# Kernel tuning notes

Hardware: AMD Instinct MI355X
Metric: run time of the kernel (lower is better)

Reference implementation:

```python
import jax, jax.numpy as jnp
import numpy as np

E = 8        # num_experts
K = 2        # top_k routing
D = 1024     # d_model
F = 4096     # expert hidden (ffn) dim
EPS = 1e-5


def _layernorm(h, g, b):
    # h: [E, T, C]; g, b: [E, C]
    mu = h.mean(axis=-1, keepdims=True)
    var = ((h - mu) ** 2).mean(axis=-1, keepdims=True)
    return (h - mu) * jax.lax.rsqrt(var + EPS) * g[:, None, :] + b[:, None, :]


def setup_inputs() -> dict:
    key = jax.random.key(0)
    ks = jax.random.split(key, 8)
    B, S = 2, 2048
    x = jax.random.normal(ks[0], (B, S, D), dtype=jnp.float32)
    Wr = jax.random.normal(ks[1], (D, E), dtype=jnp.float32) / np.sqrt(D)
    br = jnp.zeros((E,), dtype=jnp.float32)
    W1 = jax.random.normal(ks[2], (E, D, F), dtype=jnp.float32) / np.sqrt(D)
    b1 = jnp.zeros((E, F), dtype=jnp.float32)
    g1 = jnp.ones((E, F), dtype=jnp.float32)
    be1 = jnp.zeros((E, F), dtype=jnp.float32)
    W2 = jax.random.normal(ks[3], (E, F, D), dtype=jnp.float32) / np.sqrt(F)
    b2 = jnp.zeros((E, D), dtype=jnp.float32)
    g2 = jnp.ones((E, D), dtype=jnp.float32)
    be2 = jnp.zeros((E, D), dtype=jnp.float32)
    return {"x": x, "Wr": Wr, "br": br, "W1": W1, "b1": b1, "g1": g1,
            "be1": be1, "W2": W2, "b2": b2, "g2": g2, "be2": be2}


def reference(x, Wr, br, W1, b1, g1, be1, W2, b2, g2, be2):
    B, S, _ = x.shape
    xt = x.reshape(-1, D)                       # [T, D] token matrix
    # --- router + sampler: top-k softmax probs, renormalized over the k slots
    logits = xt @ Wr + br                       # [T, E]
    p = jax.nn.softmax(logits, axis=-1)
    probs, idx = jax.lax.top_k(p, K)            # [T, K]
    probs = probs / probs.sum(axis=-1, keepdims=True)
    # --- experts layer 1: Linear -> relu -> LayerNorm, per expert
    h = jnp.einsum('td,edf->etf', xt, W1) + b1[:, None, :]   # [E, T, F]
    h = _layernorm(jax.nn.relu(h), g1, be1)
    # --- experts layer 2: Linear -> relu -> LayerNorm
    y = jnp.einsum('etf,efd->etd', h, W2) + b2[:, None, :]   # [E, T, D]
    y = _layernorm(jax.nn.relu(y), g2, be2)
    # --- weighted scatter-combine: gate[t,e] = sum_k 1[idx[t,k]==e] * probs[t,k]
    gate = (jax.nn.one_hot(idx, E, dtype=x.dtype) * probs[..., None]).sum(axis=1)  # [T, E]
    out = jnp.einsum('te,etd->td', gate, y)     # index_add combine, dense form
    return out.reshape(B, S, D)
```

## Files before the change

### kernel.cpp

```cpp
#include <hip/hip_runtime.h>


#define E_N 8
#define TOPK 2
#define DM 1024
#define FF 4096
#define NTOK 4096
#define NA 8192
#define LN_EPS 1e-5f
#define NBX 128

typedef __attribute__((ext_vector_type(4))) float f32x4;
typedef __attribute__((ext_vector_type(8))) short short8;

__device__ __forceinline__ unsigned short f2bf(float f) {
    unsigned int u = __builtin_bit_cast(unsigned int, f);
    u = (u + 0x7FFFu + ((u >> 16) & 1u)) >> 16;
    return (unsigned short)u;
}
__device__ __forceinline__ float bf2f(unsigned short h) {
    unsigned int u = ((unsigned int)h) << 16;
    return __builtin_bit_cast(float, u);
}
__device__ __forceinline__ void unp(unsigned int u, float& lo, float& hi) {
    lo = bf2f((unsigned short)(u & 0xffffu));
    hi = bf2f((unsigned short)(u >> 16));
}
__device__ __forceinline__ unsigned int pk(float lo, float hi) {
    return (unsigned int)f2bf(lo) | ((unsigned int)f2bf(hi) << 16);
}

__device__ __forceinline__ void gload16(const unsigned short* g, unsigned short* lds) {
    __builtin_amdgcn_global_load_lds(
        (const __attribute__((address_space(1))) unsigned int*)g,
        (__attribute__((address_space(3))) unsigned int*)lds, 16, 0, 0);
}

__device__ __forceinline__ void stage_tile(const float* __restrict__ s, int sld,
                                           float* buf) {
    int tid = threadIdx.x;
    int wv = tid >> 6, lane = tid & 63;
    int kl = lane >> 5;
    int n = (lane & 31) * 4;
#pragma unroll
    for (int i = 0; i < 8; i++) {
        int j = wv * 8 + i;
        int k = j * 2 + kl;
        gload16((const unsigned short*)(s + (size_t)k * sld + n),
                (unsigned short*)(buf + j * 256));
    }
}

__device__ __forceinline__ void emit_tile(const float* __restrict__ tile,
                                          unsigned short* __restrict__ out) {
    int tid = threadIdx.x;
    int r = tid >> 1, gh = (tid & 1) * 4;
    const float* col = tile + r;
    unsigned int ov[16];
#pragma unroll
    for (int i = 0; i < 4; i++) {
        int kb = ((gh + i) ^ (r & 7)) << 3;
#pragma unroll
        for (int ee = 0; ee < 8; ee += 2)
            ov[i * 4 + (ee >> 1)] = pk(col[(kb + ee) * 128], col[(kb + ee + 1) * 128]);
    }
    unsigned short* dp = out + (size_t)r * 64 + gh * 8;
#pragma unroll
    for (int i = 0; i < 4; i++)
        *(uint4*)(dp + i * 8) = *(uint4*)&ov[i * 4];
}


__global__ __launch_bounds__(256) void k_prep(
        const float* __restrict__ W1, const float* __restrict__ W2,
        unsigned short* __restrict__ W1T, unsigned short* __restrict__ W2T,
        const float* __restrict__ x, const float* __restrict__ Wr,
        const float* __restrict__ br, unsigned short* __restrict__ xb,
        int* __restrict__ topk_idx, float* __restrict__ topk_p)
{
    __shared__ float tile[2][64 * 128];
    int bid = blockIdx.x;
    int tid = threadIdx.x;

    if (bid >= 2048) {
        int blk = bid - 2048;
        int wv = tid >> 6, lane = tid & 63;
        int t = blk * 4 + wv;
        const float* xr = x + (size_t)t * DM;
        unsigned short* xbr = xb + (size_t)t * DM;
        float4 xv[4];
#pragma unroll
        for (int p = 0; p < 4; p++)
            xv[p] = *(const float4*)(xr + p * 256 + lane * 4);
#pragma unroll
        for (int p = 0; p < 4; p++) {
            uint2 pkd; pkd.x = pk(xv[p].x, xv[p].y); pkd.y = pk(xv[p].z, xv[p].w);
            *(uint2*)(xbr + p * 256 + lane * 4) = pkd;
        }
        float a0=0,a1=0,a2=0,a3=0,a4=0,a5=0,a6=0,a7=0;
#pragma unroll
        for (int p = 0; p < 4; p++) {
            int d0 = p * 256 + lane * 4;
            float xs[4] = {xv[p].x, xv[p].y, xv[p].z, xv[p].w};
#pragma unroll
            for (int j = 0; j < 4; j++) {
                const float4* wp = (const float4*)(Wr + (d0 + j) * 8);
                float4 w0 = wp[0], w1 = wp[1];
                a0 += xs[j] * w0.x; a1 += xs[j] * w0.y; a2 += xs[j] * w0.z; a3 += xs[j] * w0.w;
                a4 += xs[j] * w1.x; a5 += xs[j] * w1.y; a6 += xs[j] * w1.z; a7 += xs[j] * w1.w;
            }
        }
#pragma unroll
        for (int off = 32; off; off >>= 1) {
            a0 += __shfl_xor(a0, off); a1 += __shfl_xor(a1, off);
            a2 += __shfl_xor(a2, off); a3 += __shfl_xor(a3, off);
            a4 += __shfl_xor(a4, off); a5 += __shfl_xor(a5, off);
            a6 += __shfl_xor(a6, off); a7 += __shfl_xor(a7, off);
        }
        if (lane == 0) {
            float l[8] = {a0 + br[0], a1 + br[1], a2 + br[2], a3 + br[3],
                          a4 + br[4], a5 + br[5], a6 + br[6], a7 + br[7]};
            int i0 = 0;
#pragma unroll
            for (int e = 1; e < 8; e++) if (l[e] > l[i0]) i0 = e;
            int i1 = (i0 == 0) ? 1 : 0;
#pragma unroll
            for (int e = 0; e < 8; e++) if (e != i0 && l[e] > l[i1]) i1 = e;
            float p1 = expf(l[i1] - l[i0]);
            float s = 1.0f + p1;
            topk_idx[2 * t]     = i0;
            topk_idx[2 * t + 1] = i1;
            topk_p[2 * t]       = 1.0f / s;
            topk_p[2 * t + 1]   = p1 / s;
        }
        return;
    }

    const float* s; unsigned short* o; int sld;
    if (bid < 1024) {
        int z = bid >> 7, nt = (bid >> 2) & 31, kt0 = (bid & 3) * 4;
        s = W1 + (size_t)z * DM * FF + (size_t)(kt0 * 64) * FF + nt * 128;
        sld = FF;
        o = W1T + (((size_t)z * 32 + nt) * 16 + kt0) * 8192;
    } else {
        int b = bid - 1024;
        int e = b >> 7, nt = (b >> 4) & 7, kt0 = (b & 15) * 4;
        s = W2 + (size_t)e * FF * DM + (size_t)(kt0 * 64) * DM + nt * 128;
        sld = DM;
        o = W2T + (((size_t)e * 8 + nt) * 64 + kt0) * 8192;
    }

    stage_tile(s, sld, tile[0]);
    __syncthreads();
#pragma unroll
    for (int q = 0; q < 4; q++) {
        if (q < 3)
            stage_tile(s + (size_t)(q + 1) * 64 * sld, sld, tile[(q + 1) & 1]);
        emit_tile(tile[q & 1], o + (size_t)q * 8192);
        if (q < 3) __syncthreads();
    }
}


__global__ __launch_bounds__(256) void k_route2(const int* __restrict__ topk_idx,
        int* __restrict__ cnt, int* __restrict__ offs,
        int* __restrict__ assign_tok, int* __restrict__ assign_e,
        int* __restrict__ slot)
{
    __shared__ int h[8], base[8];
    int tid = threadIdx.x;
    if (tid < 8) h[tid] = 0;
    __syncthreads();
    int el[32];
#pragma unroll
    for (int i = 0; i < 32; i++) {
        int idx = tid * 32 + i;
        el[i] = topk_idx[idx];
        atomicAdd(&h[el[i]], 1);
    }
    __syncthreads();
    if (tid == 0) {
        int s = 0;
        for (int e = 0; e < E_N; e++) { offs[e] = s; cnt[e] = h[e]; base[e] = s; s += h[e]; }
        offs[E_N] = s;
    }
    __syncthreads();
    if (tid < 8) h[tid] = base[tid];
    __syncthreads();
#pragma unroll
    for (int i = 0; i < 32; i++) {
        int idx = tid * 32 + i;
        int e = el[i];
        int pos = atomicAdd(&h[e], 1);
        assign_tok[pos] = idx >> 1;
        assign_e[pos] = e;
        slot[idx] = pos;
    }
}


template<bool GATHER, bool EPI>
__global__ __launch_bounds__(256, 4) void k_gemm(
    const unsigned short* __restrict__ A,
    const unsigned short* __restrict__ BT,
    const float* __restrict__ bias,
    unsigned short* __restrict__ C,
    const int* __restrict__ cnt, const int* __restrict__ offs,
    const int* __restrict__ gather_tok,
    int Kslice, int N, int ldA, int NT, int KT, int GX, int KS, size_t slicePitch)
{
    __shared__ __align__(1024) char lds[32768];

    int bid = blockIdx.x;
    int e = bid & 7;
    int lb = bid >> 3;
    int M = cnt[e];
    if (M <= 0) return;
    int off_e = offs[e];
    int nrows = (M + 127) >> 7;
    int ntiles = nrows * GX * KS;

    int tid = threadIdx.x;
    int wv = tid >> 6, lane = tid & 63;
    int lr = lane & 15, hi = lane >> 4;
    int mW = (wv >> 1) * 64, nW = (wv & 1) * 64;
    int colsw = ((lane & 7) ^ (lane >> 3)) * 8;
    int l3 = lane >> 3;
    int nt = Kslice >> 6;

    for (int t = lb; t < ntiles; t += NBX) {
        int r = t % nrows;
        int q = t / nrows;
        int xn = q % GX;
        int ks = q / GX;
        int m0 = r * 128;
        int n0 = xn * 128;
        int kbase = ks * Kslice;

        const unsigned short* aptr[4];
        const unsigned short* bptr[4];
        size_t btile = ((size_t)(e * NT + xn) * KT + (size_t)ks * nt) * 8192;
#pragma unroll
        for (int i = 0; i < 4; i++) {
            int j = wv * 4 + i;
            int rr = m0 + j * 8 + l3; rr = (rr < M) ? rr : (M - 1);
            size_t arow = GATHER ? (size_t)gather_tok[off_e + rr] : (size_t)(off_e + rr);
            aptr[i] = A + arow * (size_t)ldA + kbase + colsw;
            bptr[i] = BT + btile + j * 512 + lane * 8;
        }

        f32x4 acc[4][4];
        f32x4 zz = {0.f, 0.f, 0.f, 0.f};
#pragma unroll
        for (int mi = 0; mi < 4; mi++)
#pragma unroll
            for (int ni = 0; ni < 4; ni++) acc[mi][ni] = zz;

        for (int kt = 0; kt < nt; ++kt) {
            __syncthreads();
#pragma unroll
            for (int i = 0; i < 4; i++) {
                gload16(aptr[i] + kt * 64, (unsigned short*)(lds + (wv * 4 + i) * 1024));
                gload16(bptr[i] + (size_t)kt * 8192,
                        (unsigned short*)(lds + 16384 + (wv * 4 + i) * 1024));
            }
            __syncthreads();
#pragma unroll
            for (int kss = 0; kss < 2; kss++) {
                int cb = (kss * 64 + hi * 16) ^ ((lr & 7) << 4);
                short8 afr[4], bfr[4];
#pragma unroll
                for (int ni = 0; ni < 4; ni++)
                    bfr[ni] = *(const short8*)(lds + 16384 + (nW + ni * 16 + lr) * 128 + cb);
#pragma unroll
                for (int mi = 0; mi < 4; mi++)
                    afr[mi] = *(const short8*)(lds + (mW + mi * 16 + lr) * 128 + cb);
                __builtin_amdgcn_s_setprio(1);
#pragma unroll
                for (int mi = 0; mi < 4; mi++)
#pragma unroll
                    for (int ni = 0; ni < 4; ni++)
                        acc[mi][ni] = __builtin_amdgcn_mfma_f32_16x16x32_bf16(
                            afr[mi], bfr[ni], acc[mi][ni], 0, 0, 0);
                __builtin_amdgcn_s_setprio(0);
            }
        }

        unsigned short* Cs = C + ks * slicePitch;
        float bv[4] = {0.f, 0.f, 0.f, 0.f};
        if (EPI) {
#pragma unroll
            for (int ni = 0; ni < 4; ni++)
                bv[ni] = bias[(size_t)e * N + (n0 + nW + ni * 16 + lr)];
        }
#pragma unroll
        for (int mi = 0; mi < 4; mi++) {
            int mb = m0 + mW + mi * 16 + hi * 4;
#pragma unroll
            for (int rr = 0; rr < 4; rr++) {
                int m = mb + rr;
                if (m < M) {
                    unsigned short* crow = Cs + (size_t)(off_e + m) * N;
#pragma unroll
                    for (int ni = 0; ni < 4; ni++) {
                        float v = acc[mi][ni][rr];
                        if (EPI) v = fmaxf(v + bv[ni], 0.0f);
                        crow[n0 + nW + ni * 16 + lr] = f2bf(v);
                    }
                }
            }
        }
    }
}


__global__ __launch_bounds__(256) void k_ln1(unsigned short* __restrict__ H,
        const float* __restrict__ g, const float* __restrict__ b,
        const int* __restrict__ assign_e)
{
    size_t a = blockIdx.x;
    int e = assign_e[a];
    unsigned short* row = H + a * FF;
    int tid = threadIdx.x;
    uint4 u0 = *(const uint4*)(row + tid * 16);
    uint4 u1 = *(const uint4*)(row + tid * 16 + 8);
    float v[16];
    unp(u0.x, v[0], v[1]);  unp(u0.y, v[2], v[3]);
    unp(u0.z, v[4], v[5]);  unp(u0.w, v[6], v[7]);
    unp(u1.x, v[8], v[9]);  unp(u1.y, v[10], v[11]);
    unp(u1.z, v[12], v[13]); unp(u1.w, v[14], v[15]);
    float s = 0.f, q = 0.f;
#pragma unroll
    for (int i = 0; i < 16; i++) { s += v[i]; q += v[i] * v[i]; }
#pragma unroll
    for (int off = 32; off; off >>= 1) { s += __shfl_xor(s, off); q += __shfl_xor(q, off); }
    __shared__ float red[8];
    int wv = tid >> 6, lane = tid & 63;
    if (lane == 0) { red[wv * 2] = s; red[wv * 2 + 1] = q; }
    __syncthreads();
    s = red[0] + red[2] + red[4] + red[6];
    q = red[1] + red[3] + red[5] + red[7];
    float mu = s * (1.0f / FF);
    float var = q * (1.0f / FF) - mu * mu;
    float rstd = rsqrtf(var + LN_EPS);
    const float* gg = g + (size_t)e * FF + tid * 16;
    const float* bb = b + (size_t)e * FF + tid * 16;
    float4 G0 = *(const float4*)(gg);      float4 G1 = *(const float4*)(gg + 4);
    float4 G2 = *(const float4*)(gg + 8);  float4 G3 = *(const float4*)(gg + 12);
    float4 B0 = *(const float4*)(bb);      float4 B1 = *(const float4*)(bb + 4);
    float4 B2 = *(const float4*)(bb + 8);  float4 B3 = *(const float4*)(bb + 12);
    float gvv[16] = {G0.x,G0.y,G0.z,G0.w,G1.x,G1.y,G1.z,G1.w,G2.x,G2.y,G2.z,G2.w,G3.x,G3.y,G3.z,G3.w};
    float bvv[16] = {B0.x,B0.y,B0.z,B0.w,B1.x,B1.y,B1.z,B1.w,B2.x,B2.y,B2.z,B2.w,B3.x,B3.y,B3.z,B3.w};
#pragma unroll
    for (int i = 0; i < 16; i++) v[i] = (v[i] - mu) * rstd * gvv[i] + bvv[i];
    u0.x = pk(v[0], v[1]);  u0.y = pk(v[2], v[3]);
    u0.z = pk(v[4], v[5]);  u0.w = pk(v[6], v[7]);
    u1.x = pk(v[8], v[9]);  u1.y = pk(v[10], v[11]);
    u1.z = pk(v[12], v[13]); u1.w = pk(v[14], v[15]);
    *(uint4*)(row + tid * 16) = u0;
    *(uint4*)(row + tid * 16 + 8) = u1;
}


__global__ __launch_bounds__(256) void k_comb(const unsigned short* __restrict__ Yp,
        const float* __restrict__ g, const float* __restrict__ b2,
        const float* __restrict__ be,
        const int* __restrict__ slot, const float* __restrict__ topk_p,
        const int* __restrict__ assign_e, float* __restrict__ out)
{
    int t = blockIdx.x;
    int s0 = slot[2 * t], s1 = slot[2 * t + 1];
    float p0 = topk_p[2 * t], p1 = topk_p[2 * t + 1];
    int e0 = assign_e[s0], e1 = assign_e[s1];
    int tid = threadIdx.x;
    int d = tid * 4;
    const unsigned short* Y1 = Yp + (size_t)NA * DM;
    uint2 ua0 = *(const uint2*)(Yp + (size_t)s0 * DM + d);
    uint2 ua1 = *(const uint2*)(Y1 + (size_t)s0 * DM + d);
    uint2 ub0 = *(const uint2*)(Yp + (size_t)s1 * DM + d);
    uint2 ub1 = *(const uint2*)(Y1 + (size_t)s1 * DM + d);
    float4 bza = *(const float4*)(b2 + (size_t)e0 * DM + d);
    float4 bzb = *(const float4*)(b2 + (size_t)e1 * DM + d);
    float x0, x1, y0, y1;
    float va[4], vb[4];
    unp(ua0.x, x0, x1); unp(ua1.x, y0, y1);
    va[0] = fmaxf(x0 + y0 + bza.x, 0.f); va[1] = fmaxf(x1 + y1 + bza.y, 0.f);
    unp(ua0.y, x0, x1); unp(ua1.y, y0, y1);
    va[2] = fmaxf(x0 + y0 + bza.z, 0.f); va[3] = fmaxf(x1 + y1 + bza.w, 0.f);
    unp(ub0.x, x0, x1); unp(ub1.x, y0, y1);
    vb[0] = fmaxf(x0 + y0 + bzb.x, 0.f); vb[1] = fmaxf(x1 + y1 + bzb.y, 0.f);
    unp(ub0.y, x0, x1); unp(ub1.y, y0, y1);
    vb[2] = fmaxf(x0 + y0 + bzb.z, 0.f); vb[3] = fmaxf(x1 + y1 + bzb.w, 0.f);

    float sa = 0.f, qa = 0.f, sb = 0.f, qb = 0.f;
#pragma unroll
    for (int i = 0; i < 4; i++) {
        sa += va[i]; qa += va[i] * va[i];
        sb += vb[i]; qb += vb[i] * vb[i];
    }
#pragma unroll
    for (int off = 32; off; off >>= 1) {
        sa += __shfl_xor(sa, off); qa += __shfl_xor(qa, off);
        sb += __shfl_xor(sb, off); qb += __shfl_xor(qb, off);
    }
    __shared__ float red[16];
    int wv = tid >> 6, lane = tid & 63;
    if (lane == 0) { red[wv*4+0]=sa; red[wv*4+1]=qa; red[wv*4+2]=sb; red[wv*4+3]=qb; }
    __syncthreads();
    sa = red[0] + red[4] + red[8]  + red[12];
    qa = red[1] + red[5] + red[9]  + red[13];
    sb = red[2] + red[6] + red[10] + red[14];
    qb = red[3] + red[7] + red[11] + red[15];
    float mua = sa * (1.0f / DM), vara = qa * (1.0f / DM) - mua * mua;
    float ra = rsqrtf(vara + LN_EPS);
    float mub = sb * (1.0f / DM), varb = qb * (1.0f / DM) - mub * mub;
    float rb = rsqrtf(varb + LN_EPS);
    float4 ga  = *(const float4*)(g + (size_t)e0 * DM + d);
    float4 ba  = *(const float4*)(be + (size_t)e0 * DM + d);
    float4 gb4 = *(const float4*)(g + (size_t)e1 * DM + d);
    float4 bb4 = *(const float4*)(be + (size_t)e1 * DM + d);
    float4 o;
    o.x = p0 * ((va[0] - mua) * ra * ga.x + ba.x) + p1 * ((vb[0] - mub) * rb * gb4.x + bb4.x);
    o.y = p0 * ((va[1] - mua) * ra * ga.y + ba.y) + p1 * ((vb[1] - mub) * rb * gb4.y + bb4.y);
    o.z = p0 * ((va[2] - mua) * ra * ga.z + ba.z) + p1 * ((vb[2] - mub) * rb * gb4.z + bb4.z);
    o.w = p0 * ((va[3] - mua) * ra * ga.w + ba.w) + p1 * ((vb[3] - mub) * rb * gb4.w + bb4.w);
    *(float4*)(out + (size_t)t * DM + d) = o;
}


extern "C" void kernel_launch(void* const* d_in, const int* in_sizes, int n_in,
                              void* d_out, int out_size, void* d_ws, size_t ws_size,
                              hipStream_t stream) {
    const float* x   = (const float*)d_in[0];
    const float* Wr  = (const float*)d_in[1];
    const float* br  = (const float*)d_in[2];
    const float* W1  = (const float*)d_in[3];
    const float* b1  = (const float*)d_in[4];
    const float* g1  = (const float*)d_in[5];
    const float* be1 = (const float*)d_in[6];
    const float* W2  = (const float*)d_in[7];
    const float* b2  = (const float*)d_in[8];
    const float* g2  = (const float*)d_in[9];
    const float* be2 = (const float*)d_in[10];
    float* out = (float*)d_out;

    char* w = (char*)d_ws;
    int*   cnt        = (int*)(w);
    int*   offs       = (int*)(w + 128);
    int*   topk_idx   = (int*)(w + 512);
    float* topk_p     = (float*)(w + 512 + (32 << 10));
    int*   assign_tok = (int*)(w + 512 + (64 << 10));
    int*   assign_e   = (int*)(w + 512 + (96 << 10));
    int*   slot       = (int*)(w + 512 + (128 << 10));
    unsigned short* xb  = (unsigned short*)(w + ((size_t)1 << 20));
    unsigned short* W1T = (unsigned short*)(w + ((size_t)9 << 20));
    unsigned short* W2T = (unsigned short*)(w + ((size_t)73 << 20));
    unsigned short* Hb  = (unsigned short*)(w + ((size_t)137 << 20));
    unsigned short* Yp  = (unsigned short*)(w + ((size_t)201 << 20));

    k_prep<<<3072, 256, 0, stream>>>(
        W1, W2, W1T, W2T, x, Wr, br, xb, topk_idx, topk_p);
    k_route2<<<1, 256, 0, stream>>>(topk_idx, cnt, offs, assign_tok, assign_e, slot);
    k_gemm<true, true><<<8 * NBX, 256, 0, stream>>>(
        xb, W1T, b1, Hb, cnt, offs, assign_tok, DM, FF, DM, 32, 16, 32, 1, 0);
    k_ln1<<<NA, 256, 0, stream>>>(Hb, g1, be1, assign_e);
    k_gemm<false, false><<<8 * NBX, 256, 0, stream>>>(
        Hb, W2T, nullptr, Yp, cnt, offs, nullptr, FF / 2, DM, FF, 8, 64, 8, 2,
        (size_t)NA * DM);
    k_comb<<<NTOK, 256, 0, stream>>>(Yp, g2, b2, be2, slot, topk_p, assign_e, out);
}
```

Baseline: 333.4 us.

## Fuse W2 transpose/convert into first expert GEMM to overlap with compute

Moves the fp32-to-bf16 transposed packing of W2 out of the prep kernel and into the first grouped GEMM. Its 512 tiles per expert are interleaved evenly among that expert's GEMM tiles, so the memory-bound weight conversion can overlap with MFMA work. This shrinks the prep kernel but adds extra syncthreads, LDS reuse and divergent work inside the GEMM's persistent loop. If an expert has zero tokens, that expert's W2T is never written.

After: 346.9 us. 1.04x slower.

```diff
diff --git a/kernel.cpp b/kernel.cpp
--- a/kernel.cpp
+++ b/kernel.cpp
@@ -72,8 +72,7 @@
 
 
 __global__ __launch_bounds__(256) void k_prep(
-        const float* __restrict__ W1, const float* __restrict__ W2,
-        unsigned short* __restrict__ W1T, unsigned short* __restrict__ W2T,
+        const float* __restrict__ W1, unsigned short* __restrict__ W1T,
         const float* __restrict__ x, const float* __restrict__ Wr,
         const float* __restrict__ br, unsigned short* __restrict__ xb,
         int* __restrict__ topk_idx, float* __restrict__ topk_p)
@@ -82,8 +81,8 @@
     int bid = blockIdx.x;
     int tid = threadIdx.x;
 
-    if (bid >= 2048) {
-        int blk = bid - 2048;
+    if (bid >= 1024) {
+        int blk = bid - 1024;
         int wv = tid >> 6, lane = tid & 63;
         int t = blk * 4 + wv;
         const float* xr = x + (size_t)t * DM;
@@ -136,26 +135,16 @@
         return;
     }
 
-    const float* s; unsigned short* o; int sld;
-    if (bid < 1024) {
-        int z = bid >> 7, nt = (bid >> 2) & 31, kt0 = (bid & 3) * 4;
-        s = W1 + (size_t)z * DM * FF + (size_t)(kt0 * 64) * FF + nt * 128;
-        sld = FF;
-        o = W1T + (((size_t)z * 32 + nt) * 16 + kt0) * 8192;
-    } else {
-        int b = bid - 1024;
-        int e = b >> 7, nt = (b >> 4) & 7, kt0 = (b & 15) * 4;
-        s = W2 + (size_t)e * FF * DM + (size_t)(kt0 * 64) * DM + nt * 128;
-        sld = DM;
-        o = W2T + (((size_t)e * 8 + nt) * 64 + kt0) * 8192;
-    }
-
-    stage_tile(s, sld, tile[0]);
+    int z = bid >> 7, nt = (bid >> 2) & 31, kt0 = (bid & 3) * 4;
+    const float* s = W1 + (size_t)z * DM * FF + (size_t)(kt0 * 64) * FF + nt * 128;
+    unsigned short* o = W1T + (((size_t)z * 32 + nt) * 16 + kt0) * 8192;
+
+    stage_tile(s, FF, tile[0]);
     __syncthreads();
 #pragma unroll
     for (int q = 0; q < 4; q++) {
         if (q < 3)
-            stage_tile(s + (size_t)(q + 1) * 64 * sld, sld, tile[(q + 1) & 1]);
+            stage_tile(s + (size_t)(q + 1) * 64 * FF, FF, tile[(q + 1) & 1]);
         emit_tile(tile[q & 1], o + (size_t)q * 8192);
         if (q < 3) __syncthreads();
     }
@@ -199,7 +188,7 @@
 }
 
 
-template<bool GATHER, bool EPI>
+template<bool GATHER, bool EPI, bool FW2>
 __global__ __launch_bounds__(256, 4) void k_gemm(
     const unsigned short* __restrict__ A,
     const unsigned short* __restrict__ BT,
@@ -207,6 +196,7 @@
     unsigned short* __restrict__ C,
     const int* __restrict__ cnt, const int* __restrict__ offs,
     const int* __restrict__ gather_tok,
+    const float* __restrict__ W2src, unsigned short* __restrict__ W2dst,
     int Kslice, int N, int ldA, int NT, int KT, int GX, int KS, size_t slicePitch)
 {
     __shared__ __align__(1024) char lds[32768];
@@ -218,7 +208,9 @@
     if (M <= 0) return;
     int off_e = offs[e];
     int nrows = (M + 127) >> 7;
-    int ntiles = nrows * GX * KS;
+    int tg = nrows * GX * KS;
+    int tw = FW2 ? 512 : 0;
+    int tot = tg + tw;
 
     int tid = threadIdx.x;
     int wv = tid >> 6, lane = tid & 63;
@@ -228,9 +220,26 @@
     int l3 = lane >> 3;
     int nt = Kslice >> 6;
 
-    for (int t = lb; t < ntiles; t += NBX) {
-        int r = t % nrows;
-        int q = t / nrows;
+    for (int t = lb; t < tot; t += NBX) {
+        int ga = FW2 ? (int)(((long long)t * tg) / tot) : t;
+        if (FW2) {
+            int gb = (int)(((long long)(t + 1) * tg) / tot);
+            if (gb == ga) {
+                int wt = t - ga;
+                int nt2 = wt >> 6, kt2 = wt & 63;
+                __syncthreads();
+                stage_tile(W2src + (size_t)e * FF * DM + (size_t)(kt2 * 64) * DM + nt2 * 128,
+                           DM, (float*)lds);
+                __syncthreads();
+                emit_tile((const float*)lds,
+                          W2dst + (((size_t)e * 8 + nt2) * 64 + kt2) * 8192);
+                continue;
+            }
+        }
+
+        int g = ga;
+        int r = g % nrows;
+        int q = g / nrows;
         int xn = q % GX;
         int ks = q / GX;
         int m0 = r * 128;
@@ -458,14 +467,14 @@
     unsigned short* Hb  = (unsigned short*)(w + ((size_t)137 << 20));
     unsigned short* Yp  = (unsigned short*)(w + ((size_t)201 << 20));
 
-    k_prep<<<3072, 256, 0, stream>>>(
-        W1, W2, W1T, W2T, x, Wr, br, xb, topk_idx, topk_p);
+    k_prep<<<2048, 256, 0, stream>>>(W1, W1T, x, Wr, br, xb, topk_idx, topk_p);
     k_route2<<<1, 256, 0, stream>>>(topk_idx, cnt, offs, assign_tok, assign_e, slot);
-    k_gemm<true, true><<<8 * NBX, 256, 0, stream>>>(
-        xb, W1T, b1, Hb, cnt, offs, assign_tok, DM, FF, DM, 32, 16, 32, 1, 0);
+    k_gemm<true, true, true><<<8 * NBX, 256, 0, stream>>>(
+        xb, W1T, b1, Hb, cnt, offs, assign_tok, W2, W2T,
+        DM, FF, DM, 32, 16, 32, 1, 0);
     k_ln1<<<NA, 256, 0, stream>>>(Hb, g1, be1, assign_e);
-    k_gemm<false, false><<<8 * NBX, 256, 0, stream>>>(
-        Hb, W2T, nullptr, Yp, cnt, offs, nullptr, FF / 2, DM, FF, 8, 64, 8, 2,
-        (size_t)NA * DM);
+    k_gemm<false, false, false><<<8 * NBX, 256, 0, stream>>>(
+        Hb, W2T, nullptr, Yp, cnt, offs, nullptr, nullptr, nullptr,
+        FF / 2, DM, FF, 8, 64, 8, 2, (size_t)NA * DM);
     k_comb<<<NTOK, 256, 0, stream>>>(Yp, g2, b2, be2, slot, topk_p, assign_e, out);
 }
```
